# Performance work log

Measured on AMD Instinct MI355X. Metric: run time of the kernel, lower is better.

Reference implementation:

```python
import jax, jax.numpy as jnp
import numpy as np

M, IN_F, OUT_F = 32, 8192, 32768
ACT_QMAX = 127.0  # act_bits=8


def unpack_int4(w_packed, in_features):
    # w_packed: (out, in//2) int32 holding two int4 nibbles per byte
    lower = w_packed & 15
    upper = (w_packed >> 4) & 15
    # sign-extend 4-bit values: v - ((v & 8) << 1) maps 8..15 -> -8..-1
    lower = lower - ((lower & 8) << 1)
    upper = upper - ((upper & 8) << 1)
    w = jnp.stack([lower, upper], axis=-1).reshape(w_packed.shape[0], -1)
    return w[:, :in_features]


def setup_inputs() -> dict:
    key = jax.random.key(0)
    k1, k2, k3, k4, k5 = jax.random.split(key, 5)
    x = jax.random.normal(k1, (M, IN_F), dtype=jnp.float32)
    # random packed bytes in [0, 256): every value is a valid pair of int4 nibbles
    weight_packed = jax.random.randint(k2, (OUT_F, IN_F // 2), 0, 256, dtype=jnp.int32)
    weight_scale = jax.random.uniform(k3, (OUT_F, 1), dtype=jnp.float32) * 0.01 + 1e-4
    act_scale = jax.random.uniform(k4, (1,), dtype=jnp.float32) * 0.1 + 0.01
    bias = jax.random.normal(k5, (OUT_F,), dtype=jnp.float32)
    return {"x": x, "weight_packed": weight_packed, "weight_scale": weight_scale,
            "act_scale": act_scale, "bias": bias}


def reference(x, weight_packed, weight_scale, act_scale, bias):
    # 1) static input quantization (round + clamp to int8 range, kept in fp32)
    x_q = jnp.clip(jnp.round(x / act_scale), -ACT_QMAX, ACT_QMAX)
    # 2) unpack int4 weights and emulate GEMM in fp32 (as the original does)
    w = unpack_int4(weight_packed, x.shape[-1]).astype(jnp.float32)  # (out, in)
    y_q = jnp.einsum('mi,oi->mo', x_q, w)  # (M, out)
    # 3) dequant: act_scale * per-channel weight_scale, then bias
    y = y_q * (act_scale * weight_scale.T)  # weight_scale.T: (1, out)
    y = y + bias[None, :]
    return y
```

## Files before the change

### kernel.cpp

```cpp
#include <hip/hip_runtime.h>
#include <stdint.h>


#define M_DIM  32
#define IN_FEAT 8192
#define OUT_FEAT 32768
#define KSPLIT 4
#define KSLICE (IN_FEAT / KSPLIT)
#define NITER  (KSLICE / 64)

typedef __attribute__((ext_vector_type(4))) int   i32x4;
typedef __attribute__((ext_vector_type(4))) float f32x4;

__global__ __launch_bounds__(256) void quant_kernel(
    const float* __restrict__ x,
    const float* __restrict__ act_scale,
    char* __restrict__ xq) {
  const int t  = blockIdx.x * blockDim.x + threadIdx.x;
  const int m  = t >> 10;
  const int g8 = t & 1023;
  const int k0 = g8 << 3;
  const int blk = k0 >> 6;
  const int g   = (k0 >> 3) & 7;
  const int pos = blk * 64 + ((g < 4) ? g * 16 : (g - 4) * 16 + 8);

  const float s = act_scale[0];
  const f32x4 v0 = *(const f32x4*)(x + (size_t)m * IN_FEAT + k0);
  const f32x4 v1 = *(const f32x4*)(x + (size_t)m * IN_FEAT + k0 + 4);
  int r0 = 0, r1 = 0;
#pragma unroll
  for (int j = 0; j < 4; ++j) {
    float qa = fminf(fmaxf(rintf(v0[j] / s), -127.0f), 127.0f);
    float qb = fminf(fmaxf(rintf(v1[j] / s), -127.0f), 127.0f);
    r0 |= ((int)qa & 0xFF) << (8 * j);
    r1 |= ((int)qb & 0xFF) << (8 * j);
  }
  int* dst = (int*)(xq + (size_t)m * IN_FEAT + pos);
  dst[0] = r0;
  dst[1] = r1;
}

__global__ __launch_bounds__(256) void gemm_kernel(
    const char* __restrict__ xq,
    const int*  __restrict__ wp,
    int* __restrict__ partial)
{
  const int lane = threadIdx.x & 63;
  const int wave = threadIdx.x >> 6;
  const int l15  = lane & 15;
  const int krow = lane >> 4;

  const int kslice = blockIdx.x & (KSPLIT - 1);
  const int nblk   = blockIdx.x >> 2;
  const int n      = (nblk << 6) + (wave << 4) + l15;
  const int kbase  = kslice * KSLICE;

  const i32x4* a0p = (const i32x4*)(xq + (size_t)l15        * IN_FEAT + kbase);
  const i32x4* a1p = (const i32x4*)(xq + (size_t)(l15 + 16) * IN_FEAT + kbase);
  const i32x4* bp  = (const i32x4*)((const char*)(wp + (size_t)n * (IN_FEAT / 2))
                                    + (size_t)kbase * 2);

  i32x4 acc0 = {0, 0, 0, 0};
  i32x4 acc1 = {0, 0, 0, 0};

  i32x4 w_lo = __builtin_nontemporal_load(&bp[krow]);
  i32x4 w_hi = __builtin_nontemporal_load(&bp[4 + krow]);
  i32x4 a0   = a0p[krow];
  i32x4 a1   = a1p[krow];

#pragma unroll 2
  for (int i = 0; i < NITER; ++i) {
    const int ip = (i + 1 < NITER) ? (i + 1) : (NITER - 1);
    i32x4 w_lo_n = __builtin_nontemporal_load(&bp[ip * 8 + krow]);
    i32x4 w_hi_n = __builtin_nontemporal_load(&bp[ip * 8 + 4 + krow]);
    i32x4 a0_n   = a0p[ip * 4 + krow];
    i32x4 a1_n   = a1p[ip * 4 + krow];

    int b0  = w_lo[0] | (w_lo[1] << 8) | (w_lo[2] << 16) | (w_lo[3] << 24);
    int b1  = w_hi[0] | (w_hi[1] << 8) | (w_hi[2] << 16) | (w_hi[3] << 24);
    int lo0 = (b0 << 4) & 0xF0F0F0F0;
    int hi0 =  b0       & 0xF0F0F0F0;
    int lo1 = (b1 << 4) & 0xF0F0F0F0;
    int hi1 =  b1       & 0xF0F0F0F0;
    i32x4 bfrag;
    bfrag[0] = __builtin_amdgcn_perm(hi0, lo0, 0x05010400);
    bfrag[1] = __builtin_amdgcn_perm(hi0, lo0, 0x07030602);
    bfrag[2] = __builtin_amdgcn_perm(hi1, lo1, 0x05010400);
    bfrag[3] = __builtin_amdgcn_perm(hi1, lo1, 0x07030602);

    acc0 = __builtin_amdgcn_mfma_i32_16x16x64_i8(a0, bfrag, acc0, 0, 0, 0);
    acc1 = __builtin_amdgcn_mfma_i32_16x16x64_i8(a1, bfrag, acc1, 0, 0, 0);

    w_lo = w_lo_n; w_hi = w_hi_n; a0 = a0_n; a1 = a1_n;
  }

  int* pout = partial + (size_t)kslice * (M_DIM * OUT_FEAT);
  const int m0 = krow * 4;
#pragma unroll
  for (int r = 0; r < 4; ++r) {
    __builtin_nontemporal_store(acc0[r], &pout[(size_t)(m0 + r)      * OUT_FEAT + n]);
    __builtin_nontemporal_store(acc1[r], &pout[(size_t)(m0 + r + 16) * OUT_FEAT + n]);
  }
}

__global__ __launch_bounds__(256) void reduce_kernel(
    const int*   __restrict__ partial,
    const float* __restrict__ wscale,
    const float* __restrict__ act_scale,
    const float* __restrict__ bias,
    float* __restrict__ out)
{
  const int t  = blockIdx.x * blockDim.x + threadIdx.x;
  const int m  = t >> 13;
  const int n4 = (t & 8191) << 2;
  const size_t off = (size_t)m * OUT_FEAT + n4;

  i32x4 s = *(const i32x4*)(partial + off);
#pragma unroll
  for (int k = 1; k < KSPLIT; ++k)
    s += *(const i32x4*)(partial + (size_t)k * (M_DIM * OUT_FEAT) + off);

  const float as = act_scale[0] * (1.0f / 16.0f);
  f32x4 ws = *(const f32x4*)(wscale + n4);
  f32x4 bs = *(const f32x4*)(bias + n4);
  f32x4 r;
#pragma unroll
  for (int j = 0; j < 4; ++j)
    r[j] = (float)s[j] * (as * ws[j]) + bs[j];
  *(f32x4*)(out + off) = r;
}

extern "C" void kernel_launch(void* const* d_in, const int* in_sizes, int n_in,
                              void* d_out, int out_size, void* d_ws, size_t ws_size,
                              hipStream_t stream) {
  const float* x      = (const float*)d_in[0];
  const int*   wp     = (const int*)  d_in[1];
  const float* wscale = (const float*)d_in[2];
  const float* ascale = (const float*)d_in[3];
  const float* bias   = (const float*)d_in[4];
  float* out = (float*)d_out;

  int*  partial = (int*)d_ws;
  char* xq      = (char*)d_ws + (size_t)KSPLIT * M_DIM * OUT_FEAT * sizeof(int);

  quant_kernel<<<(M_DIM * IN_FEAT / 8) / 256, 256, 0, stream>>>(x, ascale, xq);
  gemm_kernel<<<(OUT_FEAT / 64) * KSPLIT, 256, 0, stream>>>(xq, wp, partial);
  reduce_kernel<<<(M_DIM * OUT_FEAT / 4) / 256, 256, 0, stream>>>(partial, wscale, ascale, bias, out);
}
```

Measured before the change: 716.1 us.

## Fuse split-K reduction and dequant epilogue into GEMM via shared-memory reduce

Each block now covers 16 output columns, with its four waves taking the four K slices, instead of spreading K slices across blocks. The partial sums are reduced in shared memory and wave 0 applies the scale and bias and writes the output directly. This removes the separate reduce kernel, the global partial-sum buffer and its round trip through memory. In exchange, the final output stores are narrower per block and three of the four waves sit idle during the epilogue.

```diff
diff --git a/kernel.cpp b/kernel.cpp
--- a/kernel.cpp
+++ b/kernel.cpp
@@ -5,8 +5,7 @@
 #define M_DIM  32
 #define IN_FEAT 8192
 #define OUT_FEAT 32768
-#define KSPLIT 4
-#define KSLICE (IN_FEAT / KSPLIT)
+#define KSLICE (IN_FEAT / 4)
 #define NITER  (KSLICE / 64)
 
 typedef __attribute__((ext_vector_type(4))) int   i32x4;
@@ -41,19 +40,20 @@
 }
 
 __global__ __launch_bounds__(256) void gemm_kernel(
-    const char* __restrict__ xq,
-    const int*  __restrict__ wp,
-    int* __restrict__ partial)
+    const char*  __restrict__ xq,
+    const int*   __restrict__ wp,
+    const float* __restrict__ wscale,
+    const float* __restrict__ act_scale,
+    const float* __restrict__ bias,
+    float* __restrict__ out)
 {
   const int lane = threadIdx.x & 63;
   const int wave = threadIdx.x >> 6;
   const int l15  = lane & 15;
   const int krow = lane >> 4;
 
-  const int kslice = blockIdx.x & (KSPLIT - 1);
-  const int nblk   = blockIdx.x >> 2;
-  const int n      = (nblk << 6) + (wave << 4) + l15;
-  const int kbase  = kslice * KSLICE;
+  const int n     = (blockIdx.x << 4) + l15;
+  const int kbase = wave * KSLICE;
 
   const i32x4* a0p = (const i32x4*)(xq + (size_t)l15        * IN_FEAT + kbase);
   const i32x4* a1p = (const i32x4*)(xq + (size_t)(l15 + 16) * IN_FEAT + kbase);
@@ -94,40 +94,29 @@
     w_lo = w_lo_n; w_hi = w_hi_n; a0 = a0_n; a1 = a1_n;
   }
 
-  int* pout = partial + (size_t)kslice * (M_DIM * OUT_FEAT);
-  const int m0 = krow * 4;
+  __shared__ int red[4][64][9];
 #pragma unroll
   for (int r = 0; r < 4; ++r) {
-    __builtin_nontemporal_store(acc0[r], &pout[(size_t)(m0 + r)      * OUT_FEAT + n]);
-    __builtin_nontemporal_store(acc1[r], &pout[(size_t)(m0 + r + 16) * OUT_FEAT + n]);
+    red[wave][lane][r]     = acc0[r];
+    red[wave][lane][r + 4] = acc1[r];
   }
-}
+  __syncthreads();
 
-__global__ __launch_bounds__(256) void reduce_kernel(
-    const int*   __restrict__ partial,
-    const float* __restrict__ wscale,
-    const float* __restrict__ act_scale,
-    const float* __restrict__ bias,
-    float* __restrict__ out)
-{
-  const int t  = blockIdx.x * blockDim.x + threadIdx.x;
-  const int m  = t >> 13;
-  const int n4 = (t & 8191) << 2;
-  const size_t off = (size_t)m * OUT_FEAT + n4;
-
-  i32x4 s = *(const i32x4*)(partial + off);
+  if (wave == 0) {
+    const float as = act_scale[0] * (1.0f / 16.0f);
+    const float sc = as * wscale[n];
+    const float bs = bias[n];
+    const int m0 = krow * 4;
 #pragma unroll
-  for (int k = 1; k < KSPLIT; ++k)
-    s += *(const i32x4*)(partial + (size_t)k * (M_DIM * OUT_FEAT) + off);
-
-  const float as = act_scale[0] * (1.0f / 16.0f);
-  f32x4 ws = *(const f32x4*)(wscale + n4);
-  f32x4 bs = *(const f32x4*)(bias + n4);
-  f32x4 r;
-#pragma unroll
-  for (int j = 0; j < 4; ++j)
-    r[j] = (float)s[j] * (as * ws[j]) + bs[j];
-  *(f32x4*)(out + off) = r;
+    for (int r = 0; r < 4; ++r) {
+      int s0 = red[0][lane][r]     + red[1][lane][r]
+             + red[2][lane][r]     + red[3][lane][r];
+      int s1 = red[0][lane][r + 4] + red[1][lane][r + 4]
+             + red[2][lane][r + 4] + red[3][lane][r + 4];
+      out[(size_t)(m0 + r)      * OUT_FEAT + n] = (float)s0 * sc + bs;
+      out[(size_t)(m0 + r + 16) * OUT_FEAT + n] = (float)s1 * sc + bs;
+    }
+  }
 }
 
 extern "C" void kernel_launch(void* const* d_in, const int* in_sizes, int n_in,
@@ -140,10 +129,8 @@
   const float* bias   = (const float*)d_in[4];
   float* out = (float*)d_out;
 
-  int*  partial = (int*)d_ws;
-  char* xq      = (char*)d_ws + (size_t)KSPLIT * M_DIM * OUT_FEAT * sizeof(int);
+  char* xq = (char*)d_ws;
 
   quant_kernel<<<(M_DIM * IN_FEAT / 8) / 256, 256, 0, stream>>>(x, ascale, xq);
-  gemm_kernel<<<(OUT_FEAT / 64) * KSPLIT, 256, 0, stream>>>(xq, wp, partial);
-  reduce_kernel<<<(M_DIM * OUT_FEAT / 4) / 256, 256, 0, stream>>>(partial, wscale, ascale, bias, out);
+  gemm_kernel<<<OUT_FEAT / 16, 256, 0, stream>>>(xq, wp, wscale, ascale, bias, out);
 }
```

Result: no change. 710.2 us (-0.8%).
